# Performance work log

Measured on AMD Instinct MI355X. Metric: run time of the kernel, lower is better.

## Reference

```python
import jax, jax.numpy as jnp
import numpy as np


def setup_inputs() -> dict:
    key = jax.random.key(0)
    k1, k2, k3 = jax.random.split(key, 3)
    B, S, D, V, C = 32, 2048, 512, 32000, 2
    tokens = jax.random.randint(k1, (B, S), 0, V, dtype=jnp.int64)
    emb_table = jax.random.normal(k2, (V, D), dtype=jnp.float32) * 0.02
    cls_w = jax.random.normal(k3, (C, D), dtype=jnp.float32) * 0.02
    cls_b = jnp.zeros((C,), dtype=jnp.float32)
    return {"tokens": tokens, "emb_table": emb_table, "cls_w": cls_w, "cls_b": cls_b}


def reference(tokens, emb_table, cls_w, cls_b):
    # Embedding lookup: [B,S,D]
    x = emb_table[tokens]
    # Unscaled self-attention (no 1/sqrt(d), no mask applied, as in source)
    scores = jnp.einsum('bsd,btd->bst', x, x)       # [B,S,S]
    attn = jax.nn.softmax(scores, axis=-1)
    out = jnp.einsum('bst,btd->bsd', attn, x)       # [B,S,D]
    # pool_type == 'select': take first token
    pooled = out[:, 0, :]                            # [B,D]
    logits = pooled @ cls_w.T + cls_b                # [B,C]
    return logits
```

## Files before the change

kernel.cpp:

```cpp
#include <hip/hip_runtime.h>
#include <math.h>

#define BB 32
#define SS 2048
#define DD 512
#define TW 16
#define NCHUNK 32

__global__ __launch_bounds__(256) void attn_pass1(
    const int* __restrict__ tokens, const float* __restrict__ emb,
    float* __restrict__ pacc, float* __restrict__ pm, float* __restrict__ pl)
{
    const int b     = blockIdx.x;
    const int chunk = blockIdx.y;
    const int tid   = threadIdx.x;
    const int wave  = tid >> 6;
    const int lane  = tid & 63;

    const int qtok = tokens[(size_t)b * SS];
    const float4* q4 = (const float4*)(emb + (size_t)qtok * DD);
    const float4 qa = q4[lane * 2];
    const float4 qb = q4[lane * 2 + 1];

    const int tbase = chunk * (4 * TW) + wave * TW;
    int mytok = 0;
    if (lane < TW) mytok = tokens[(size_t)b * SS + tbase + lane];

    float m = -INFINITY, l = 0.f;
    float a0=0.f,a1=0.f,a2=0.f,a3=0.f,a4=0.f,a5=0.f,a6=0.f,a7=0.f;

    int tok0 = __shfl(mytok, 0);
    const float4* r4 = (const float4*)(emb + (size_t)tok0 * DD);
    float4 ra = r4[lane * 2];
    float4 rb = r4[lane * 2 + 1];

#pragma unroll
    for (int i = 0; i < TW; ++i) {
        float4 na = ra, nb = rb;
        if (i + 1 < TW) {
            int ntok = __shfl(mytok, i + 1);
            const float4* n4 = (const float4*)(emb + (size_t)ntok * DD);
            na = n4[lane * 2];
            nb = n4[lane * 2 + 1];
        }

        float s = qa.x*ra.x + qa.y*ra.y + qa.z*ra.z + qa.w*ra.w
                + qb.x*rb.x + qb.y*rb.y + qb.z*rb.z + qb.w*rb.w;
#pragma unroll
        for (int off = 32; off > 0; off >>= 1)
            s += __shfl_xor(s, off);

        float mn    = fmaxf(m, s);
        float alpha = expf(m - mn);
        float p     = expf(s - mn);
        l  = l * alpha + p;
        a0 = a0 * alpha + p * ra.x;  a1 = a1 * alpha + p * ra.y;
        a2 = a2 * alpha + p * ra.z;  a3 = a3 * alpha + p * ra.w;
        a4 = a4 * alpha + p * rb.x;  a5 = a5 * alpha + p * rb.y;
        a6 = a6 * alpha + p * rb.z;  a7 = a7 * alpha + p * rb.w;
        m  = mn;

        ra = na; rb = nb;
    }

    __shared__ float smax[4], ssum[4];
    __shared__ float sacc[4 * DD];
    {
        float* dst = &sacc[wave * DD + lane * 8];
        dst[0]=a0; dst[1]=a1; dst[2]=a2; dst[3]=a3;
        dst[4]=a4; dst[5]=a5; dst[6]=a6; dst[7]=a7;
        if (lane == 0) { smax[wave] = m; ssum[wave] = l; }
    }
    __syncthreads();

    const float M  = fmaxf(fmaxf(smax[0], smax[1]), fmaxf(smax[2], smax[3]));
    const float e0 = expf(smax[0] - M), e1 = expf(smax[1] - M);
    const float e2 = expf(smax[2] - M), e3 = expf(smax[3] - M);

    if (tid == 0) {
        pm[b * NCHUNK + chunk] = M;
        pl[b * NCHUNK + chunk] = e0*ssum[0] + e1*ssum[1] + e2*ssum[2] + e3*ssum[3];
    }
#pragma unroll
    for (int d = tid; d < DD; d += 256) {
        float v = e0*sacc[0*DD + d] + e1*sacc[1*DD + d]
                + e2*sacc[2*DD + d] + e3*sacc[3*DD + d];
        pacc[((size_t)(b * NCHUNK + chunk)) * DD + d] = v;
    }
}

__global__ __launch_bounds__(256) void attn_merge(
    const float* __restrict__ pacc, const float* __restrict__ pm,
    const float* __restrict__ pl,   const float* __restrict__ cls_w,
    const float* __restrict__ cls_b, float* __restrict__ out)
{
    const int b   = blockIdx.x;
    const int tid = threadIdx.x;

    __shared__ float sm[NCHUNK], sl[NCHUNK];
    if (tid < NCHUNK) {
        sm[tid] = pm[b * NCHUNK + tid];
        sl[tid] = pl[b * NCHUNK + tid];
    }
    __syncthreads();

    float M = -INFINITY;
#pragma unroll
    for (int i = 0; i < NCHUNK; ++i) M = fmaxf(M, sm[i]);
    float e[NCHUNK];
    float L = 0.f;
#pragma unroll
    for (int i = 0; i < NCHUNK; ++i) { e[i] = expf(sm[i] - M); L += e[i] * sl[i]; }
    const float invL = 1.0f / L;

    float part0 = 0.f, part1 = 0.f;
#pragma unroll
    for (int d = tid; d < DD; d += 256) {
        float v = 0.f;
#pragma unroll
        for (int i = 0; i < NCHUNK; ++i)
            v += e[i] * pacc[((size_t)(b * NCHUNK + i)) * DD + d];
        v *= invL;
        part0 += v * cls_w[d];
        part1 += v * cls_w[DD + d];
    }

    __shared__ float r0[256], r1[256];
    r0[tid] = part0; r1[tid] = part1;
    __syncthreads();
#pragma unroll
    for (int s2 = 128; s2 > 0; s2 >>= 1) {
        if (tid < s2) { r0[tid] += r0[tid + s2]; r1[tid] += r1[tid + s2]; }
        __syncthreads();
    }
    if (tid == 0) {
        out[b * 2 + 0] = r0[0] + cls_b[0];
        out[b * 2 + 1] = r1[0] + cls_b[1];
    }
}

extern "C" void kernel_launch(void* const* d_in, const int* in_sizes, int n_in,
                              void* d_out, int out_size, void* d_ws, size_t ws_size,
                              hipStream_t stream)
{
    const int*   tokens = (const int*)  d_in[0];
    const float* emb    = (const float*)d_in[1];
    const float* cls_w  = (const float*)d_in[2];
    const float* cls_b  = (const float*)d_in[3];
    float*       out    = (float*)d_out;

    float* pacc = (float*)d_ws;
    float* pm   = pacc + (size_t)BB * NCHUNK * DD;
    float* pl   = pm   + (size_t)BB * NCHUNK;

    dim3 g1(BB, NCHUNK);
    attn_pass1<<<g1, 256, 0, stream>>>(tokens, emb, pacc, pm, pl);
    attn_merge<<<BB, 256, 0, stream>>>(pacc, pm, pl, cls_w, cls_b, out);
}
```

Measured before the change: 111.2 us.

## Stage embedding rows into LDS via async global_load_lds and drop online-softmax max

Pass 1 now gathers embedding rows with global_load_lds into a double-buffered LDS stage, four rows per step, and waits on vmcnt so the next group's loads overlap compute on the current one. It processes four scores at a time, batching the shuffle reductions. It also drops the running-max rescaling and uses plain exp(s), which removes the max tracking and the pm buffer from both kernels. The risk is overflow if scores grow large. That holds for the 0.02-scaled embeddings, where scores stay small, but it is an approximation tied to the input scale.

```diff
diff --git a/kernel.cpp b/kernel.cpp
--- a/kernel.cpp
+++ b/kernel.cpp
@@ -1,116 +1,132 @@
 #include <hip/hip_runtime.h>
 #include <math.h>
+#include <stdint.h>
 
 #define BB 32
 #define SS 2048
 #define DD 512
-#define TW 16
-#define NCHUNK 32
+#define SR 4
+#define NST 4
+#define WPB 4
+#define TPERBLK (WPB * NST * SR)
+#define NCHUNK (SS / TPERBLK)
+
+typedef const __attribute__((address_space(1))) uint32_t* gas_u32;
+typedef __attribute__((address_space(3))) uint32_t* las_u32;
+
+__device__ __forceinline__ void stage_row(const float* __restrict__ g,
+                                          float* l, int lane) {
+    __builtin_amdgcn_global_load_lds((gas_u32)(g + lane * 4),
+                                     (las_u32)(l), 16, 0, 0);
+    __builtin_amdgcn_global_load_lds((gas_u32)(g + 256 + lane * 4),
+                                     (las_u32)(l + 256), 16, 0, 0);
+}
 
 __global__ __launch_bounds__(256) void attn_pass1(
     const int* __restrict__ tokens, const float* __restrict__ emb,
-    float* __restrict__ pacc, float* __restrict__ pm, float* __restrict__ pl)
+    float* __restrict__ pacc, float* __restrict__ pl)
 {
+    __shared__ float stage[WPB][2][SR][DD];
+
     const int b     = blockIdx.x;
     const int chunk = blockIdx.y;
     const int tid   = threadIdx.x;
     const int wave  = tid >> 6;
     const int lane  = tid & 63;
+    const int tok_base = b * SS + chunk * TPERBLK + wave * (NST * SR);
 
-    const int qtok = tokens[(size_t)b * SS];
-    const float4* q4 = (const float4*)(emb + (size_t)qtok * DD);
-    const float4 qa = q4[lane * 2];
-    const float4 qb = q4[lane * 2 + 1];
-
-    const int tbase = chunk * (4 * TW) + wave * TW;
-    int mytok = 0;
-    if (lane < TW) mytok = tokens[(size_t)b * SS + tbase + lane];
-
-    float m = -INFINITY, l = 0.f;
-    float a0=0.f,a1=0.f,a2=0.f,a3=0.f,a4=0.f,a5=0.f,a6=0.f,a7=0.f;
-
-    int tok0 = __shfl(mytok, 0);
-    const float4* r4 = (const float4*)(emb + (size_t)tok0 * DD);
-    float4 ra = r4[lane * 2];
-    float4 rb = r4[lane * 2 + 1];
+    const int qtok = tokens[b * SS];
+    const float4* q4 = (const float4*)(emb + (size_t)qtok * DD) + lane * 2;
+    const float4 qa = q4[0], qb = q4[1];
 
 #pragma unroll
-    for (int i = 0; i < TW; ++i) {
-        float4 na = ra, nb = rb;
-        if (i + 1 < TW) {
-            int ntok = __shfl(mytok, i + 1);
-            const float4* n4 = (const float4*)(emb + (size_t)ntok * DD);
-            na = n4[lane * 2];
-            nb = n4[lane * 2 + 1];
+    for (int r = 0; r < SR; ++r) {
+        int tk = tokens[tok_base + r];
+        stage_row(emb + (size_t)tk * DD, &stage[wave][0][r][0], lane);
+    }
+
+    float  l  = 0.f;
+    float4 aa = {0.f, 0.f, 0.f, 0.f}, ab = {0.f, 0.f, 0.f, 0.f};
+
+#pragma unroll
+    for (int k = 0; k < NST; ++k) {
+        if (k + 1 < NST) {
+#pragma unroll
+            for (int r = 0; r < SR; ++r) {
+                int tk = tokens[tok_base + (k + 1) * SR + r];
+                stage_row(emb + (size_t)tk * DD, &stage[wave][(k + 1) & 1][r][0], lane);
+            }
+            __builtin_amdgcn_s_waitcnt(0x0F78);
+        } else {
+            __builtin_amdgcn_s_waitcnt(0x0F70);
         }
 
-        float s = qa.x*ra.x + qa.y*ra.y + qa.z*ra.z + qa.w*ra.w
-                + qb.x*rb.x + qb.y*rb.y + qb.z*rb.z + qb.w*rb.w;
+        const float* bufb = &stage[wave][k & 1][0][0];
+        float4 ra[SR], rb[SR];
+        float  s[SR];
 #pragma unroll
-        for (int off = 32; off > 0; off >>= 1)
-            s += __shfl_xor(s, off);
-
-        float mn    = fmaxf(m, s);
-        float alpha = expf(m - mn);
-        float p     = expf(s - mn);
-        l  = l * alpha + p;
-        a0 = a0 * alpha + p * ra.x;  a1 = a1 * alpha + p * ra.y;
-        a2 = a2 * alpha + p * ra.z;  a3 = a3 * alpha + p * ra.w;
-        a4 = a4 * alpha + p * rb.x;  a5 = a5 * alpha + p * rb.y;
-        a6 = a6 * alpha + p * rb.z;  a7 = a7 * alpha + p * rb.w;
-        m  = mn;
-
-        ra = na; rb = nb;
+        for (int r = 0; r < SR; ++r) {
+            const float4* p4 = (const float4*)(bufb + r * DD) + lane * 2;
+            ra[r] = p4[0];
+            rb[r] = p4[1];
+        }
+#pragma unroll
+        for (int r = 0; r < SR; ++r) {
+            s[r] = qa.x*ra[r].x + qa.y*ra[r].y + qa.z*ra[r].z + qa.w*ra[r].w
+                 + qb.x*rb[r].x + qb.y*rb[r].y + qb.z*rb[r].z + qb.w*rb[r].w;
+        }
+#pragma unroll
+        for (int off = 32; off > 0; off >>= 1) {
+#pragma unroll
+            for (int r = 0; r < SR; ++r) s[r] += __shfl_xor(s[r], off);
+        }
+#pragma unroll
+        for (int r = 0; r < SR; ++r) {
+            float p = expf(s[r]);
+            l += p;
+            aa.x += p * ra[r].x;  aa.y += p * ra[r].y;
+            aa.z += p * ra[r].z;  aa.w += p * ra[r].w;
+            ab.x += p * rb[r].x;  ab.y += p * rb[r].y;
+            ab.z += p * rb[r].z;  ab.w += p * rb[r].w;
+        }
     }
 
-    __shared__ float smax[4], ssum[4];
-    __shared__ float sacc[4 * DD];
+    float* scomb = (float*)stage;
+    __syncthreads();
     {
-        float* dst = &sacc[wave * DD + lane * 8];
-        dst[0]=a0; dst[1]=a1; dst[2]=a2; dst[3]=a3;
-        dst[4]=a4; dst[5]=a5; dst[6]=a6; dst[7]=a7;
-        if (lane == 0) { smax[wave] = m; ssum[wave] = l; }
+        float* dst = scomb + wave * DD + lane * 8;
+        dst[0]=aa.x; dst[1]=aa.y; dst[2]=aa.z; dst[3]=aa.w;
+        dst[4]=ab.x; dst[5]=ab.y; dst[6]=ab.z; dst[7]=ab.w;
+        if (lane == 0) scomb[WPB * DD + wave] = l;
     }
     __syncthreads();
 
-    const float M  = fmaxf(fmaxf(smax[0], smax[1]), fmaxf(smax[2], smax[3]));
-    const float e0 = expf(smax[0] - M), e1 = expf(smax[1] - M);
-    const float e2 = expf(smax[2] - M), e3 = expf(smax[3] - M);
-
     if (tid == 0) {
-        pm[b * NCHUNK + chunk] = M;
-        pl[b * NCHUNK + chunk] = e0*ssum[0] + e1*ssum[1] + e2*ssum[2] + e3*ssum[3];
+        pl[b * NCHUNK + chunk] = scomb[WPB*DD+0] + scomb[WPB*DD+1]
+                               + scomb[WPB*DD+2] + scomb[WPB*DD+3];
     }
 #pragma unroll
     for (int d = tid; d < DD; d += 256) {
-        float v = e0*sacc[0*DD + d] + e1*sacc[1*DD + d]
-                + e2*sacc[2*DD + d] + e3*sacc[3*DD + d];
-        pacc[((size_t)(b * NCHUNK + chunk)) * DD + d] = v;
+        pacc[((size_t)(b * NCHUNK + chunk)) * DD + d] =
+            scomb[0*DD + d] + scomb[1*DD + d] + scomb[2*DD + d] + scomb[3*DD + d];
     }
 }
 
 __global__ __launch_bounds__(256) void attn_merge(
-    const float* __restrict__ pacc, const float* __restrict__ pm,
-    const float* __restrict__ pl,   const float* __restrict__ cls_w,
-    const float* __restrict__ cls_b, float* __restrict__ out)
+    const float* __restrict__ pacc, const float* __restrict__ pl,
+    const float* __restrict__ cls_w, const float* __restrict__ cls_b,
+    float* __restrict__ out)
 {
     const int b   = blockIdx.x;
     const int tid = threadIdx.x;
 
-    __shared__ float sm[NCHUNK], sl[NCHUNK];
-    if (tid < NCHUNK) {
-        sm[tid] = pm[b * NCHUNK + tid];
-        sl[tid] = pl[b * NCHUNK + tid];
-    }
+    __shared__ float sl[NCHUNK];
+    if (tid < NCHUNK) sl[tid] = pl[b * NCHUNK + tid];
     __syncthreads();
 
-    float M = -INFINITY;
-#pragma unroll
-    for (int i = 0; i < NCHUNK; ++i) M = fmaxf(M, sm[i]);
-    float e[NCHUNK];
     float L = 0.f;
 #pragma unroll
-    for (int i = 0; i < NCHUNK; ++i) { e[i] = expf(sm[i] - M); L += e[i] * sl[i]; }
+    for (int i = 0; i < NCHUNK; ++i) L += sl[i];
     const float invL = 1.0f / L;
 
     float part0 = 0.f, part1 = 0.f;
@@ -119,7 +135,7 @@
         float v = 0.f;
 #pragma unroll
         for (int i = 0; i < NCHUNK; ++i)
-            v += e[i] * pacc[((size_t)(b * NCHUNK + i)) * DD + d];
+            v += pacc[((size_t)(b * NCHUNK + i)) * DD + d];
         v *= invL;
         part0 += v * cls_w[d];
         part1 += v * cls_w[DD + d];
@@ -150,10 +166,9 @@
     float*       out    = (float*)d_out;
 
     float* pacc = (float*)d_ws;
-    float* pm   = pacc + (size_t)BB * NCHUNK * DD;
-    float* pl   = pm   + (size_t)BB * NCHUNK;
+    float* pl   = pacc + (size_t)BB * NCHUNK * DD;
 
     dim3 g1(BB, NCHUNK);
-    attn_pass1<<<g1, 256, 0, stream>>>(tokens, emb, pacc, pm, pl);
-    attn_merge<<<BB, 256, 0, stream>>>(pacc, pm, pl, cls_w, cls_b, out);
+    attn_pass1<<<g1, 256, 0, stream>>>(tokens, emb, pacc, pl);
+    attn_merge<<<BB, 256, 0, stream>>>(pacc, pl, cls_w, cls_b, out);
 }
```

Result: no change. 113.0 us (+1.6%).
